# Performance work log

Hardware: AMD Instinct MI355X
Metric: run time of the kernel (lower is better)

The kernel has to match this reference:

```python
import jax, jax.numpy as jnp
import numpy as np

N = 16384
E = 524288
F_IN, F_HID, F_OUT = 128, 256, 128
EPS = 1e-5


def setup_inputs() -> dict:
    key = jax.random.key(0)
    ks = jax.random.split(key, 8)
    x = jax.random.normal(ks[0], (N, F_IN), dtype=jnp.float32)
    edge_index = jax.random.randint(ks[1], (2, E), 0, N, dtype=jnp.int64)
    edge_weight = jax.random.uniform(ks[2], (E,), dtype=jnp.float32)
    # Linear params stored as [in, out] (y = x @ W + b; same math as torch Linear)
    W1_w = jax.random.normal(ks[3], (F_IN, F_HID), dtype=jnp.float32) / np.sqrt(F_IN)
    W1_b = jnp.zeros((F_HID,), dtype=jnp.float32)
    W2_w = jax.random.normal(ks[4], (F_HID, F_OUT), dtype=jnp.float32) / np.sqrt(F_HID)
    W2_b = jnp.zeros((F_OUT,), dtype=jnp.float32)
    ln_g = jnp.ones((F_HID,), dtype=jnp.float32)
    ln_b = jnp.zeros((F_HID,), dtype=jnp.float32)
    return {"x": x, "edge_index": edge_index, "edge_weight": edge_weight,
            "W1_w": W1_w, "W1_b": W1_b, "W2_w": W2_w, "W2_b": W2_b,
            "ln_g": ln_g, "ln_b": ln_b}


def _layernorm(h, g, b):
    mu = jnp.mean(h, axis=-1, keepdims=True)
    var = jnp.var(h, axis=-1, keepdims=True)
    return (h - mu) * jax.lax.rsqrt(var + EPS) * g + b


def reference(x, edge_index, edge_weight, W1_w, W1_b, W2_w, W2_b, ln_g, ln_b):
    n = x.shape[0]
    adj = jnp.zeros((n, n), dtype=x.dtype).at[edge_index[0], edge_index[1]].set(edge_weight)
    adj = adj + jnp.eye(n, dtype=x.dtype)
    degree = jnp.clip(adj.sum(axis=1, keepdims=True), 1.0, None)
    adj = adj / degree
    h = jnp.matmul(adj, x) @ W1_w + W1_b          # [N, F_HID]
    h = jax.nn.relu(_layernorm(h, ln_g, ln_b))
    # dropout is identity in eval mode
    out = jnp.matmul(adj, h) @ W2_w + W2_b        # [N, F_OUT]
    return out
```

## Files before the change

### kernel.cpp

```cpp
#include <hip/hip_runtime.h>

#define N_NODES 16384
#define F_IN    128
#define F_HID   256
#define F_OUT   128
#define LN_EPS  1e-5f
#define CAP     128
#define HSTR    264

typedef __attribute__((ext_vector_type(8))) short bf16x8;
typedef __attribute__((ext_vector_type(4))) float f32x4;
typedef unsigned short u16;

__device__ __forceinline__ u16 bf16rne(float f) {
    unsigned u = __float_as_uint(f);
    unsigned r = (u + 0x7fffu + ((u >> 16) & 1u)) >> 16;
    return (u16)r;
}
__device__ __forceinline__ float bf_lo(unsigned v) { return __uint_as_float(v << 16); }

__global__ void prelude_kernel(const float* __restrict__ x, u16* __restrict__ xb,
                               const float* __restrict__ W1, u16* __restrict__ W1t,
                               const float* __restrict__ W2, u16* __restrict__ W2t,
                               int* __restrict__ cur, const unsigned* __restrict__ ei,
                               int* __restrict__ mode) {
    int b = blockIdx.x, t = threadIdx.x;
    if (b < 2048) {
        int i = (b * 256 + t) * 4;
        float4 v = *(const float4*)&x[i];
        ushort4 o;
        o.x = bf16rne(v.x); o.y = bf16rne(v.y); o.z = bf16rne(v.z); o.w = bf16rne(v.w);
        *(ushort4*)&xb[i] = o;
    } else if (b < 2176) {
        int id = (b - 2048) * 256 + t;
        int n = id >> 7, k = id & 127;
        W1t[id] = bf16rne(W1[(size_t)k * F_HID + n]);
    } else if (b < 2304) {
        int id = (b - 2176) * 256 + t;
        int n = id >> 8, k = id & 255;
        W2t[id] = bf16rne(W2[(size_t)k * F_OUT + n]);
    } else if (b < 2368) {
        cur[(b - 2304) * 256 + t] = 0;
    } else {
        __shared__ int nz;
        if (t == 0) nz = 0;
        __syncthreads();
        for (int it = 0; it < 4; ++it) {
            int idx = 2 * (t + it * 256) + 1;
            if (ei[idx] != 0u) nz = 1;
        }
        __syncthreads();
        if (t == 0) *mode = (nz == 0) ? 1 : 0;
    }
}

__global__ void fill_kernel(const void* __restrict__ ei, const int* __restrict__ mode,
                            int* __restrict__ cur, int2* __restrict__ ed, int E) {
    int base = blockIdx.x * 1024 + threadIdx.x;
    int m = *mode;
#pragma unroll
    for (int u = 0; u < 4; ++u) {
        int e = base + u * 256;
        if (e >= E) continue;
        int r, c;
        if (m) {
            const long long* p = (const long long*)ei;
            r = (int)p[e]; c = (int)p[e + E];
        } else {
            const int* p = (const int*)ei;
            r = p[e]; c = p[e + E];
        }
        if (((unsigned)r | (unsigned)c) >= N_NODES) continue;
        int pos = atomicAdd(&cur[r], 1);
        if (pos < CAP) ed[r * CAP + pos] = make_int2(c, e);
    }
}

__global__ void dedupe_kernel(const float* __restrict__ ew, int* __restrict__ cur,
                              const int2* __restrict__ ed, unsigned* __restrict__ edp,
                              float* __restrict__ invdeg) {
    __shared__ int scol[4][CAP];
    __shared__ int seid[4][CAP];
    int wave = threadIdx.x >> 6, lane = threadIdx.x & 63;
    int r = blockIdx.x * 4 + wave;
    int d = cur[r];
    if (d > CAP) d = CAP;
    int dpad = (d + 15) & ~15;
    if (dpad > CAP) dpad = CAP;
    const int2* row = ed + r * CAP;
    for (int i = lane; i < d; i += 64) {
        int2 e = row[i];
        scol[wave][i] = e.x;
        seid[wave][i] = e.y;
    }
    __syncthreads();
    float wsum = 0.0f;
    unsigned* orow = edp + r * CAP;
    for (int i = lane; i < dpad; i += 64) {
        if (i < d) {
            int myc = scol[wave][i], mye = seid[wave][i];
            bool kill = false;
            for (int j = 0; j < d; ++j)
                if (scol[wave][j] == myc && seid[wave][j] > mye) { kill = true; break; }
            float w = kill ? 0.0f : ew[mye];
            wsum += w;
            orow[i] = ((unsigned)bf16rne(w) << 16) | (unsigned)myc;
        } else {
            orow[i] = (unsigned)r;
        }
    }
    for (int off = 32; off; off >>= 1) wsum += __shfl_xor(wsum, off, 64);
    if (lane == 0) {
        invdeg[r] = 1.0f / (1.0f + wsum);
        cur[r] = dpad;
    }
}

__launch_bounds__(256)
__global__ void spmm_kernel(const u16* __restrict__ xb, const int* __restrict__ cur,
                            const unsigned* __restrict__ edp, const float* __restrict__ invdeg,
                            const float* __restrict__ bias, void* __restrict__ outp,
                            int out_bf16) {
    int wid = threadIdx.x >> 6, lane = threadIdx.x & 63;
    int half = blockIdx.x & 1;
    int r = __builtin_amdgcn_readfirstlane((blockIdx.x >> 1) * 4 + wid);
    int hb = half * 64;
    int sidx = r * F_IN + hb + lane;
    float acc = bf_lo((unsigned)xb[sidx]);
    int dpad = cur[r];
    const unsigned* rowp = edp + r * CAP;
    for (int j = 0; j < dpad; j += 16) {
        unsigned dsc[16];
#pragma unroll
        for (int u = 0; u < 16; ++u) dsc[u] = rowp[j + u];
#pragma unroll
        for (int u = 0; u < 16; ++u) {
            int col = (int)(dsc[u] & 0xffffu);
            float w = __uint_as_float(dsc[u] & 0xffff0000u);
            unsigned v = (unsigned)xb[col * F_IN + hb + lane];
            acc += w * bf_lo(v);
        }
    }
    float o = acc * invdeg[r];
    if (bias) o += bias[hb + lane];
    if (out_bf16) ((u16*)outp)[sidx] = bf16rne(o);
    else          ((float*)outp)[sidx] = o;
}

__launch_bounds__(256)
__global__ void mlp_mfma_kernel(const u16* __restrict__ h0b,
                                const u16* __restrict__ W1t,
                                const u16* __restrict__ W2t,
                                const float* __restrict__ b1,
                                const float* __restrict__ ln_g, const float* __restrict__ ln_b,
                                u16* __restrict__ h2b) {
    __shared__ u16 Hs[4][16 * HSTR];
    int t = threadIdx.x;
    int wid = t >> 6, lane = t & 63;
    int lnid = lane & 15, quad = lane >> 4;
    int R = blockIdx.x * 64 + wid * 16;
    u16* H = Hs[wid];

    bf16x8 a[4];
#pragma unroll
    for (int ch = 0; ch < 4; ++ch)
        a[ch] = *(const bf16x8*)&h0b[(size_t)(R + lnid) * F_IN + ch * 32 + quad * 8];
    f32x4 acc[16];
#pragma unroll
    for (int ct = 0; ct < 16; ++ct) {
        f32x4 c = {0.0f, 0.0f, 0.0f, 0.0f};
        const u16* wrow = &W1t[(size_t)(ct * 16 + lnid) * F_IN];
#pragma unroll
        for (int ch = 0; ch < 4; ++ch) {
            bf16x8 b = *(const bf16x8*)&wrow[ch * 32 + quad * 8];
            c = __builtin_amdgcn_mfma_f32_16x16x32_bf16(a[ch], b, c, 0, 0, 0);
        }
        acc[ct] = c;
    }
    float s[4] = {0, 0, 0, 0}, q[4] = {0, 0, 0, 0};
#pragma unroll
    for (int ct = 0; ct < 16; ++ct) {
        float bv = b1[ct * 16 + lnid];
#pragma unroll
        for (int r = 0; r < 4; ++r) {
            float v = acc[ct][r] + bv;
            acc[ct][r] = v;
            s[r] += v; q[r] += v * v;
        }
    }
#pragma unroll
    for (int r = 0; r < 4; ++r)
        for (int off = 1; off < 16; off <<= 1) {
            s[r] += __shfl_xor(s[r], off, 64);
            q[r] += __shfl_xor(q[r], off, 64);
        }
    float mean[4], rinv[4];
#pragma unroll
    for (int r = 0; r < 4; ++r) {
        mean[r] = s[r] * (1.0f / F_HID);
        float var = q[r] * (1.0f / F_HID) - mean[r] * mean[r];
        rinv[r] = rsqrtf(var + LN_EPS);
    }
#pragma unroll
    for (int ct = 0; ct < 16; ++ct) {
        int c = ct * 16 + lnid;
        float g = ln_g[c], bb = ln_b[c];
#pragma unroll
        for (int r = 0; r < 4; ++r) {
            float v = fmaxf((acc[ct][r] - mean[r]) * rinv[r] * g + bb, 0.0f);
            H[(quad * 4 + r) * HSTR + c] = bf16rne(v);
        }
    }
    __syncthreads();

    bf16x8 a2[8];
#pragma unroll
    for (int ch = 0; ch < 8; ++ch)
        a2[ch] = *(const bf16x8*)&H[lnid * HSTR + ch * 32 + quad * 8];
#pragma unroll
    for (int ct = 0; ct < 8; ++ct) {
        f32x4 c = {0.0f, 0.0f, 0.0f, 0.0f};
        const u16* wrow = &W2t[(size_t)(ct * 16 + lnid) * F_HID];
#pragma unroll
        for (int ch = 0; ch < 8; ++ch) {
            bf16x8 b = *(const bf16x8*)&wrow[ch * 32 + quad * 8];
            c = __builtin_amdgcn_mfma_f32_16x16x32_bf16(a2[ch], b, c, 0, 0, 0);
        }
#pragma unroll
        for (int r = 0; r < 4; ++r)
            H[(quad * 4 + r) * 132 + ct * 16 + lnid] = bf16rne(c[r]);
    }
    __syncthreads();

#pragma unroll
    for (int p = 0; p < 8; ++p) {
        int flat = p * 64 + lane;
        int m = flat >> 5, cg = flat & 31;
        *(ushort4*)&h2b[(size_t)(R + m) * F_OUT + cg * 4] =
            *(const ushort4*)&H[m * 132 + cg * 4];
    }
}

extern "C" void kernel_launch(void* const* d_in, const int* in_sizes, int n_in,
                              void* d_out, int out_size, void* d_ws, size_t ws_size,
                              hipStream_t stream) {
    const float* x   = (const float*)d_in[0];
    const void*  ei  = d_in[1];
    const float* ew  = (const float*)d_in[2];
    const float* W1  = (const float*)d_in[3];
    const float* b1  = (const float*)d_in[4];
    const float* W2  = (const float*)d_in[5];
    const float* b2  = (const float*)d_in[6];
    const float* lng = (const float*)d_in[7];
    const float* lnb = (const float*)d_in[8];
    float* out = (float*)d_out;
    int E = in_sizes[2];

    char* w = (char*)d_ws;
    size_t off = 0;
    auto take = [&](size_t bytes) -> char* {
        char* p = w + off;
        off += (bytes + 255) & ~(size_t)255;
        return p;
    };
    int*      cur    = (int*)take((size_t)N_NODES * 4);
    float*    invdeg = (float*)take((size_t)N_NODES * 4);
    int2*     ed     = (int2*)take((size_t)N_NODES * CAP * 8);
    unsigned* edp    = (unsigned*)take((size_t)N_NODES * CAP * 4);
    u16* xb  = (u16*)take((size_t)N_NODES * F_IN * 2);
    u16* h0b = (u16*)take((size_t)N_NODES * F_IN * 2);
    u16* h2b = (u16*)take((size_t)N_NODES * F_OUT * 2);
    u16* W1t = (u16*)take((size_t)F_IN * F_HID * 2);
    u16* W2t = (u16*)take((size_t)F_HID * F_OUT * 2);
    int* mode = (int*)take(4);

    prelude_kernel<<<2369, 256, 0, stream>>>(x, xb, W1, W1t, W2, W2t, cur,
                                             (const unsigned*)ei, mode);
    fill_kernel<<<(E + 1023) / 1024, 256, 0, stream>>>(ei, mode, cur, ed, E);
    dedupe_kernel<<<N_NODES / 4, 256, 0, stream>>>(ew, cur, ed, edp, invdeg);
    spmm_kernel<<<N_NODES / 2, 256, 0, stream>>>(xb, cur, edp, invdeg, nullptr, h0b, 1);
    mlp_mfma_kernel<<<N_NODES / 64, 256, 0, stream>>>(h0b, W1t, W2t, b1, lng, lnb, h2b);
    spmm_kernel<<<N_NODES / 2, 256, 0, stream>>>(h2b, cur, edp, invdeg, b2, out, 0);
}
```

Before: 195.6 us.

## Fuse dedupe with first SpMM and vectorize SpMM to two features per lane

The dedupe kernel now also performs the first sparse aggregation, reading packed edge descriptors from shared memory instead of re-reading them from global memory, which removes one kernel launch and a pass over the edge list. Both SpMM paths now process two bf16 features per lane with 32-bit loads, so one wave covers a full row instead of splitting it across two blocks. Neighbor loads are issued in a batch before the FMAs for more memory-level parallelism, and nontemporal loads and stores are used for streaming edge and output data. The second SpMM now always reads the bias pointer, which is only safe because a bias is always passed.

```diff
diff --git a/kernel.cpp b/kernel.cpp
--- a/kernel.cpp
+++ b/kernel.cpp
@@ -10,19 +10,23 @@
 
 typedef __attribute__((ext_vector_type(8))) short bf16x8;
 typedef __attribute__((ext_vector_type(4))) float f32x4;
+typedef __attribute__((ext_vector_type(2))) float f32x2;
 typedef unsigned short u16;
+typedef unsigned int u32;
+typedef unsigned long long u64;
 
 __device__ __forceinline__ u16 bf16rne(float f) {
     unsigned u = __float_as_uint(f);
     unsigned r = (u + 0x7fffu + ((u >> 16) & 1u)) >> 16;
     return (u16)r;
 }
-__device__ __forceinline__ float bf_lo(unsigned v) { return __uint_as_float(v << 16); }
+__device__ __forceinline__ float bf_lo(u32 v) { return __uint_as_float(v << 16); }
+__device__ __forceinline__ float bf_hi(u32 v) { return __uint_as_float(v & 0xffff0000u); }
 
 __global__ void prelude_kernel(const float* __restrict__ x, u16* __restrict__ xb,
                                const float* __restrict__ W1, u16* __restrict__ W1t,
                                const float* __restrict__ W2, u16* __restrict__ W2t,
-                               int* __restrict__ cur, const unsigned* __restrict__ ei,
+                               int* __restrict__ cur, const u32* __restrict__ ei,
                                int* __restrict__ mode) {
     int b = blockIdx.x, t = threadIdx.x;
     if (b < 2048) {
@@ -65,86 +69,128 @@
         int r, c;
         if (m) {
             const long long* p = (const long long*)ei;
-            r = (int)p[e]; c = (int)p[e + E];
+            r = (int)__builtin_nontemporal_load(&p[e]);
+            c = (int)__builtin_nontemporal_load(&p[e + E]);
         } else {
             const int* p = (const int*)ei;
-            r = p[e]; c = p[e + E];
+            r = __builtin_nontemporal_load(&p[e]);
+            c = __builtin_nontemporal_load(&p[e + E]);
         }
         if (((unsigned)r | (unsigned)c) >= N_NODES) continue;
         int pos = atomicAdd(&cur[r], 1);
-        if (pos < CAP) ed[r * CAP + pos] = make_int2(c, e);
-    }
-}
-
-__global__ void dedupe_kernel(const float* __restrict__ ew, int* __restrict__ cur,
-                              const int2* __restrict__ ed, unsigned* __restrict__ edp,
-                              float* __restrict__ invdeg) {
+        if (pos < CAP) {
+            u64 pk = (u64)(u32)c | ((u64)(u32)e << 32);
+            __builtin_nontemporal_store(pk, (u64*)&ed[r * CAP + pos]);
+        }
+    }
+}
+
+__launch_bounds__(256)
+__global__ void dd1_kernel(const float* __restrict__ ew, int* __restrict__ cur,
+                           const int2* __restrict__ ed, u32* __restrict__ edp,
+                           float* __restrict__ invdeg, const u32* __restrict__ xb,
+                           u32* __restrict__ h0b) {
     __shared__ int scol[4][CAP];
     __shared__ int seid[4][CAP];
-    int wave = threadIdx.x >> 6, lane = threadIdx.x & 63;
-    int r = blockIdx.x * 4 + wave;
+    __shared__ u32 spk[4][CAP];
+    int wid = threadIdx.x >> 6, lane = threadIdx.x & 63;
+    int r = blockIdx.x * 4 + wid;
     int d = cur[r];
     if (d > CAP) d = CAP;
     int dpad = (d + 15) & ~15;
     if (dpad > CAP) dpad = CAP;
-    const int2* row = ed + r * CAP;
+
+    const u64* row64 = (const u64*)(ed + r * CAP);
     for (int i = lane; i < d; i += 64) {
-        int2 e = row[i];
-        scol[wave][i] = e.x;
-        seid[wave][i] = e.y;
+        u64 pk = __builtin_nontemporal_load(&row64[i]);
+        scol[wid][i] = (int)(u32)pk;
+        seid[wid][i] = (int)(u32)(pk >> 32);
     }
     __syncthreads();
+
     float wsum = 0.0f;
-    unsigned* orow = edp + r * CAP;
+    u32* orow = edp + r * CAP;
     for (int i = lane; i < dpad; i += 64) {
+        u32 pk;
         if (i < d) {
-            int myc = scol[wave][i], mye = seid[wave][i];
+            int myc = scol[wid][i], mye = seid[wid][i];
             bool kill = false;
             for (int j = 0; j < d; ++j)
-                if (scol[wave][j] == myc && seid[wave][j] > mye) { kill = true; break; }
+                if (scol[wid][j] == myc && seid[wid][j] > mye) { kill = true; break; }
             float w = kill ? 0.0f : ew[mye];
             wsum += w;
-            orow[i] = ((unsigned)bf16rne(w) << 16) | (unsigned)myc;
+            pk = ((u32)bf16rne(w) << 16) | (u32)myc;
         } else {
-            orow[i] = (unsigned)r;
-        }
+            pk = (u32)r;
+        }
+        spk[wid][i] = pk;
+        __builtin_nontemporal_store(pk, &orow[i]);
     }
     for (int off = 32; off; off >>= 1) wsum += __shfl_xor(wsum, off, 64);
-    if (lane == 0) {
-        invdeg[r] = 1.0f / (1.0f + wsum);
-        cur[r] = dpad;
-    }
+    float inv = 1.0f / (1.0f + wsum);
+    if (lane == 0) { invdeg[r] = inv; cur[r] = dpad; }
+    __syncthreads();
+
+    float ax, ay;
+    {
+        u32 self = xb[r * 64 + lane];
+        ax = bf_lo(self); ay = bf_hi(self);
+    }
+    const uint4* pk4 = (const uint4*)spk[wid];
+    for (int j = 0; j < dpad; j += 16) {
+        uint4 q[4];
+#pragma unroll
+        for (int u = 0; u < 4; ++u) q[u] = pk4[(j >> 2) + u];
+        u32 dsc[16];
+#pragma unroll
+        for (int u = 0; u < 4; ++u) {
+            dsc[4 * u] = q[u].x; dsc[4 * u + 1] = q[u].y;
+            dsc[4 * u + 2] = q[u].z; dsc[4 * u + 3] = q[u].w;
+        }
+        u32 v[16];
+#pragma unroll
+        for (int u = 0; u < 16; ++u) v[u] = xb[(dsc[u] & 0xffffu) * 64 + lane];
+#pragma unroll
+        for (int u = 0; u < 16; ++u) {
+            float w = __uint_as_float(dsc[u] & 0xffff0000u);
+            ax += w * bf_lo(v[u]);
+            ay += w * bf_hi(v[u]);
+        }
+    }
+    float ox = ax * inv, oy = ay * inv;
+    u32 pk = ((u32)bf16rne(oy) << 16) | (u32)bf16rne(ox);
+    __builtin_nontemporal_store(pk, &h0b[r * 64 + lane]);
 }
 
 __launch_bounds__(256)
-__global__ void spmm_kernel(const u16* __restrict__ xb, const int* __restrict__ cur,
-                            const unsigned* __restrict__ edp, const float* __restrict__ invdeg,
-                            const float* __restrict__ bias, void* __restrict__ outp,
-                            int out_bf16) {
+__global__ void spmm2_kernel(const u32* __restrict__ xb, const int* __restrict__ cur,
+                             const u32* __restrict__ edp, const float* __restrict__ invdeg,
+                             const float* __restrict__ bias, float* __restrict__ outp) {
     int wid = threadIdx.x >> 6, lane = threadIdx.x & 63;
-    int half = blockIdx.x & 1;
-    int r = __builtin_amdgcn_readfirstlane((blockIdx.x >> 1) * 4 + wid);
-    int hb = half * 64;
-    int sidx = r * F_IN + hb + lane;
-    float acc = bf_lo((unsigned)xb[sidx]);
+    int r = __builtin_amdgcn_readfirstlane(blockIdx.x * 4 + wid);
     int dpad = cur[r];
-    const unsigned* rowp = edp + r * CAP;
+    const u32* rowp = edp + r * CAP;
+    u32 self = xb[r * 64 + lane];
+    float ax = bf_lo(self), ay = bf_hi(self);
     for (int j = 0; j < dpad; j += 16) {
-        unsigned dsc[16];
+        u32 dsc[16];
 #pragma unroll
         for (int u = 0; u < 16; ++u) dsc[u] = rowp[j + u];
+        u32 v[16];
+#pragma unroll
+        for (int u = 0; u < 16; ++u) v[u] = xb[(dsc[u] & 0xffffu) * 64 + lane];
 #pragma unroll
         for (int u = 0; u < 16; ++u) {
-            int col = (int)(dsc[u] & 0xffffu);
             float w = __uint_as_float(dsc[u] & 0xffff0000u);
-            unsigned v = (unsigned)xb[col * F_IN + hb + lane];
-            acc += w * bf_lo(v);
-        }
-    }
-    float o = acc * invdeg[r];
-    if (bias) o += bias[hb + lane];
-    if (out_bf16) ((u16*)outp)[sidx] = bf16rne(o);
-    else          ((float*)outp)[sidx] = o;
+            ax += w * bf_lo(v[u]);
+            ay += w * bf_hi(v[u]);
+        }
+    }
+    float inv = invdeg[r];
+    f32x2 o;
+    o.x = ax * inv + bias[2 * lane];
+    o.y = ay * inv + bias[2 * lane + 1];
+    __builtin_nontemporal_store(o, (f32x2*)&outp[r * 128 + 2 * lane]);
 }
 
 __launch_bounds__(256)
@@ -263,10 +309,10 @@
         off += (bytes + 255) & ~(size_t)255;
         return p;
     };
-    int*      cur    = (int*)take((size_t)N_NODES * 4);
-    float*    invdeg = (float*)take((size_t)N_NODES * 4);
-    int2*     ed     = (int2*)take((size_t)N_NODES * CAP * 8);
-    unsigned* edp    = (unsigned*)take((size_t)N_NODES * CAP * 4);
+    int*   cur    = (int*)take((size_t)N_NODES * 4);
+    float* invdeg = (float*)take((size_t)N_NODES * 4);
+    int2*  ed     = (int2*)take((size_t)N_NODES * CAP * 8);
+    u32*   edp    = (u32*)take((size_t)N_NODES * CAP * 4);
     u16* xb  = (u16*)take((size_t)N_NODES * F_IN * 2);
     u16* h0b = (u16*)take((size_t)N_NODES * F_IN * 2);
     u16* h2b = (u16*)take((size_t)N_NODES * F_OUT * 2);
@@ -275,10 +321,11 @@
     int* mode = (int*)take(4);
 
     prelude_kernel<<<2369, 256, 0, stream>>>(x, xb, W1, W1t, W2, W2t, cur,
-                                             (const unsigned*)ei, mode);
+                                             (const u32*)ei, mode);
     fill_kernel<<<(E + 1023) / 1024, 256, 0, stream>>>(ei, mode, cur, ed, E);
-    dedupe_kernel<<<N_NODES / 4, 256, 0, stream>>>(ew, cur, ed, edp, invdeg);
-    spmm_kernel<<<N_NODES / 2, 256, 0, stream>>>(xb, cur, edp, invdeg, nullptr, h0b, 1);
+    dd1_kernel<<<N_NODES / 4, 256, 0, stream>>>(ew, cur, ed, edp, invdeg,
+                                                (const u32*)xb, (u32*)h0b);
     mlp_mfma_kernel<<<N_NODES / 64, 256, 0, stream>>>(h0b, W1t, W2t, b1, lng, lnb, h2b);
-    spmm_kernel<<<N_NODES / 2, 256, 0, stream>>>(h2b, cur, edp, invdeg, b2, out, 0);
-}
+    spmm2_kernel<<<N_NODES / 4, 256, 0, stream>>>((const u32*)h2b, cur, edp, invdeg,
+                                                  b2, out);
+}
```

After: 195.9 us. No clear change (+0.2%).
